# Performance work log

Measured on AMD Instinct MI355X. Metric: run time of the kernel, lower is better.

## Reference

```python
import jax, jax.numpy as jnp
import numpy as np

# Conv config (matches init_kwargs)
STRIDE = (1, 1)
PADDING = ((1, 1), (1, 1))
B, CIN, COUT, H, W = 16, 128, 256, 56, 56
KH, KW = 3, 3


def _conv(x, w):
    # NCHW input, OIHW kernel, zeros padding mode
    return jax.lax.conv_general_dilated(
        x, w, window_strides=STRIDE, padding=PADDING,
        dimension_numbers=("NCHW", "OIHW", "NCHW"))


def setup_inputs() -> dict:
    key = jax.random.key(0)
    ks = jax.random.split(key, 6)
    x = jax.random.normal(ks[0], (B, CIN, H, W), dtype=jnp.float32)
    # quantized weight: integer-valued floats (output of module.Q.quantize)
    weight = jnp.round(jax.random.normal(ks[1], (COUT, CIN, KH, KW), dtype=jnp.float32) * 4.0)
    act_s = jnp.asarray(0.0625, dtype=jnp.float32)   # exp2(log_act_s)
    act_q = jnp.asarray(16.0, dtype=jnp.float32)     # exp2(log_act_q)
    azp = jnp.asarray(-4.0, dtype=jnp.float32)       # rounded act zero point (scaled by guard_a)
    wzp = jnp.round(jax.random.normal(ks[2], (COUT,), dtype=jnp.float32) * 2.0)
    fp_scale = (jax.random.uniform(ks[3], (1, COUT, 1, 1), dtype=jnp.float32) + 0.5) * 1e-3
    # bias_full has spatial extent [1, COUT, H_out, W_out]
    bias = jax.random.normal(ks[4], (1, COUT, H, W), dtype=jnp.float32) * 0.1
    guard_a = jnp.asarray(2.0, dtype=jnp.float32)    # 2**act_guard_bit
    guard_w = jnp.asarray(2.0, dtype=jnp.float32)    # 2**weight_guard_bit
    return {"x": x, "weight": weight, "act_s": act_s, "act_q": act_q,
            "azp": azp, "wzp": wzp, "fp_scale": fp_scale, "bias": bias,
            "guard_a": guard_a, "guard_w": guard_w}


def reference(x, weight, act_s, act_q, azp, wzp, fp_scale, bias, guard_a, guard_w):
    # 1) Activation quantization: clamp to quant range then round to integer grid.
    zp = azp * act_s / guard_a
    xq = jnp.clip(x, zp, zp + act_q - act_s)
    xq = guard_a * jnp.round((xq - zp) / act_s)
    # 2) Main integer conv with quantized weights.
    c1 = _conv(xq, weight)
    # 3) Ones-kernel conv: output is identical across all COUT channels,
    #    so compute once as channel-sum followed by a single-channel box conv.
    s = jnp.sum(xq, axis=1, keepdims=True)  # [B, 1, H, W]
    ones_k = jnp.ones((1, 1) + weight.shape[2:], dtype=x.dtype)
    c2 = _conv(s, ones_k)  # [B, 1, H_out, W_out], broadcasts over channels
    # 4) Affine dequant + spatially-varying bias epilogue.
    out = guard_w * c1 + wzp[None, :, None, None] * c2
    return out * fp_scale + bias
```

## Files before the change

kernel.cpp:

```cpp
#include <hip/hip_runtime.h>

#define B_    16
#define CIN_  128
#define COUT_ 256
#define H_    56
#define W_    56
#define YP    58
#define XP    64

typedef int   i32x4 __attribute__((ext_vector_type(4)));
typedef float f4    __attribute__((ext_vector_type(4)));

#define AS_SZ 8192
#define BH_SZ 24704

__device__ __forceinline__ void gload16(const void* g, void* l) {
    __builtin_amdgcn_global_load_lds(
        (const __attribute__((address_space(1))) unsigned int*)g,
        (__attribute__((address_space(3))) unsigned int*)l,
        16, 0, 0);
}

__global__ __launch_bounds__(256) void k_prep(
    const float* __restrict__ x, const float* __restrict__ w,
    const float* __restrict__ p_act_s, const float* __restrict__ p_act_q,
    const float* __restrict__ p_azp,  const float* __restrict__ p_guard_a,
    signed char* __restrict__ xqU, signed char* __restrict__ wt,
    float* __restrict__ s_pad, float* __restrict__ Wsum)
{
    int t = threadIdx.x;
    int blk = blockIdx.x;

    if (blk < 928) {
        int b = blk / YP, y = blk - b * YP;
        __shared__ signed char shq[W_ * 144];
        signed char* orow = xqU + (size_t)blk * XP * CIN_;

        if (y == 0 || y == YP - 1) {
            i32x4 pv = {(int)0x80808080, (int)0x80808080,
                        (int)0x80808080, (int)0x80808080};
            *(i32x4*)(orow + t * 32)      = pv;
            *(i32x4*)(orow + t * 32 + 16) = pv;
            if (t < XP) s_pad[(size_t)blk * XP + t] = 0.0f;
            return;
        }
        int h = y - 1;
        float act_s = p_act_s[0], act_q = p_act_q[0];
        float azp = p_azp[0], ga = p_guard_a[0];
        float zp = azp * act_s / ga;
        float hi = zp + act_q - act_s;
        float inv_s = 1.0f / act_s;

        for (int i = 0; i < 28; ++i) {
            int e = i * 256 + t;
            int cin = e / 56;
            int ww = e - cin * 56;
            float v = x[(((size_t)b * CIN_ + cin) * H_ + h) * W_ + ww];
            v = fminf(fmaxf(v, zp), hi);
            float r = rintf((v - zp) * inv_s);
            float uq = rintf(ga * r * 0.5f) - 128.0f;
            shq[ww * 144 + cin] = (signed char)(int)uq;
        }
        __syncthreads();
        #pragma unroll
        for (int i = 0; i < 2; ++i) {
            int T = i * 256 + t;
            int xx = T >> 3;
            int c16 = T & 7;
            union { i32x4 v; signed char c[16]; } u;
            if (xx >= 1 && xx <= W_) {
                u.v = *(const i32x4*)(shq + (xx - 1) * 144 + c16 * 16);
            } else {
                u.v = (i32x4){(int)0x80808080, (int)0x80808080,
                              (int)0x80808080, (int)0x80808080};
            }
            *(i32x4*)(orow + (size_t)xx * CIN_ + c16 * 16) = u.v;
            int sum = 0;
            #pragma unroll
            for (int j = 0; j < 16; ++j) sum += (int)u.c[j];
            sum += __shfl_xor(sum, 1);
            sum += __shfl_xor(sum, 2);
            sum += __shfl_xor(sum, 4);
            if (c16 == 0)
                s_pad[(size_t)blk * XP + xx] = (float)(2 * sum + 32768);
        }
        return;
    }

    if (blk < 1216) {
        int o = ((blk - 928) * 256 + t) * 4;
        int tile = o >> 13;
        int m    = (o >> 6) & 127;
        int kk   = o & 63;
        int cb = tile & 1, cc = (tile >> 1) & 1, g = tile >> 2;
        int cout = cb * 128 + m;
        int cin0 = cc * 64 + kk;
        int dy = g / 3, dx = g - dy * 3;
        union { int v; signed char c[4]; } pk;
        #pragma unroll
        for (int j = 0; j < 4; ++j) {
            float v = w[(size_t)cout * 1152 + (cin0 + j) * 9 + dy * 3 + dx];
            pk.c[j] = (signed char)(int)v;
        }
        *(int*)(wt + o) = pk.v;
        return;
    }

    {
        int bw = blk - 1216;
        int cout = bw * 16 + (t >> 4);
        int part = t & 15;
        const float* base = w + (size_t)cout * 1152 + part * 72;
        float s = 0.f;
        for (int j = 0; j < 72; ++j) s += base[j];
        s += __shfl_xor(s, 1);
        s += __shfl_xor(s, 2);
        s += __shfl_xor(s, 4);
        s += __shfl_xor(s, 8);
        if (part == 0) Wsum[cout] = s;
        return;
    }
}

__global__ __launch_bounds__(256, 2) void k_gemm(
    const signed char* __restrict__ xqU,
    const signed char* __restrict__ wt,
    const float* __restrict__ s_pad,
    const float* __restrict__ Wsum,
    const float* __restrict__ wzp,
    const float* __restrict__ fps,
    const float* __restrict__ bias,
    const float* __restrict__ p_gw,
    float* __restrict__ out)
{
    __shared__ __align__(16) signed char As[2][AS_SZ];
    __shared__ __align__(16) signed char Bh[2][BH_SZ];
    __shared__ float c2s[4 * 56];

    int tid = threadIdx.x;
    int wv = tid >> 6, lane = tid & 63;
    int xl = lane & 15, q = lane >> 4;
    int p = blockIdx.x, cb = blockIdx.y;
    int b = p / 14, hp = p - b * 14;
    int h = hp * 4;
    int wm0 = (wv >> 1) * 64, wn0 = (wv & 1) * 128;

    if (tid < 224) {
        int rr = tid / 56, wp = tid - rr * 56;
        const float* sp = s_pad + ((size_t)(b * YP + h + rr)) * XP + wp;
        float a = 0.f;
        #pragma unroll
        for (int dy = 0; dy < 3; ++dy)
            #pragma unroll
            for (int dx = 0; dx < 3; ++dx)
                a += sp[dy * XP + dx];
        c2s[tid] = a;
    }

    i32x4 acc[4][8];
    #pragma unroll
    for (int mi = 0; mi < 4; ++mi)
        #pragma unroll
        for (int ni = 0; ni < 8; ++ni)
            acc[mi][ni] = (i32x4){0, 0, 0, 0};

    const signed char* xb = xqU + (size_t)(b * YP + h) * XP * CIN_;

    int a_base = (wm0 + xl) * 64 + q * 16;
    int bn_base[8];
    #pragma unroll
    for (int ni = 0; ni < 8; ++ni) {
        int n = wn0 + ni * 16 + xl;
        int rn = n >> 6, wp = n & 63;
        bn_base[ni] = (rn * XP + wp) * 64 + q * 16;
    }

    #define STAGE_A(buf_, g_, cc_)                                          \
        {                                                                   \
            const signed char* wsrc = wt + (size_t)((((g_)*2+(cc_))*2)+cb) * 8192; \
            signed char* dstb = As[buf_];                                   \
            _Pragma("unroll")                                               \
            for (int r_ = 0; r_ < 2; ++r_)                                  \
                gload16(wsrc + (r_ * 256 + tid) * 16,                       \
                        dstb + (r_ * 256 + wv * 64) * 16);                  \
        }
    #define STAGE_B(buf_, cc_)                                              \
        {                                                                   \
            signed char* dstb = Bh[buf_];                                   \
            _Pragma("unroll")                                               \
            for (int r_ = 0; r_ < 6; ++r_) {                                \
                int T_ = r_ * 256 + tid;                                    \
                int p_ = T_ & 3;                                            \
                int x_ = (T_ >> 2) & 63;                                    \
                int yy_ = T_ >> 8;                                          \
                gload16(xb + (size_t)(yy_ * XP + x_) * CIN_ + (cc_) * 64 + p_ * 16, \
                        dstb + (r_ * 256 + wv * 64) * 16);                  \
            }                                                               \
        }

    STAGE_A(0, 0, 0)
    STAGE_B(0, 0)
    __syncthreads();

    for (int i = 0; i < 18; ++i) {
        int cc = (i >= 9) ? 1 : 0;
        int g = i - cc * 9;
        if (i < 17) {
            int gn = g + 1, ccn = cc;
            if (gn == 9) { gn = 0; ccn = 1; }
            STAGE_A((i + 1) & 1, gn, ccn)
            if (gn == 0) STAGE_B(1, 1)
        }
        {
            const signed char* Ab = As[i & 1];
            const signed char* Bb = Bh[cc];
            int dy = g / 3, dx = g - dy * 3;
            int boff = dy * (XP * 64) + dx * 64;
            i32x4 af[4], bfr[8];
            #pragma unroll
            for (int mi = 0; mi < 4; ++mi)
                af[mi] = *(const i32x4*)(Ab + a_base + mi * 1024);
            #pragma unroll
            for (int ni = 0; ni < 8; ++ni)
                bfr[ni] = *(const i32x4*)(Bb + bn_base[ni] + boff);
            #pragma unroll
            for (int mi = 0; mi < 4; ++mi)
                #pragma unroll
                for (int ni = 0; ni < 8; ++ni)
                    acc[mi][ni] = __builtin_amdgcn_mfma_i32_16x16x64_i8(
                        af[mi], bfr[ni], acc[mi][ni], 0, 0, 0);
        }
        __syncthreads();
    }

    float gw = p_gw[0];
    #pragma unroll
    for (int mi = 0; mi < 4; ++mi) {
        #pragma unroll
        for (int r = 0; r < 4; ++r) {
            int cout = cb * 128 + wm0 + mi * 16 + q * 4 + r;
            float wz = wzp[cout], fs = fps[cout], ws = Wsum[cout];
            #pragma unroll
            for (int ni = 0; ni < 8; ++ni) {
                int n = wn0 + ni * 16 + xl;
                int wp = n & 63;
                if (wp < W_) {
                    int rn = n >> 6;
                    int hrow = h + rn;
                    float c1 = 2.0f * (float)acc[mi][ni][r] + 256.0f * ws;
                    float v = gw * c1 + wz * c2s[rn * 56 + wp];
                    out[(((size_t)b * COUT_ + cout) * H_ + hrow) * W_ + wp] =
                        v * fs + bias[((size_t)cout * H_ + hrow) * W_ + wp];
                }
            }
        }
    }
}

extern "C" void kernel_launch(void* const* d_in, const int* in_sizes, int n_in,
                              void* d_out, int out_size, void* d_ws, size_t ws_size,
                              hipStream_t stream)
{
    const float* x     = (const float*)d_in[0];
    const float* wht   = (const float*)d_in[1];
    const float* act_s = (const float*)d_in[2];
    const float* act_q = (const float*)d_in[3];
    const float* azp   = (const float*)d_in[4];
    const float* wzp   = (const float*)d_in[5];
    const float* fps   = (const float*)d_in[6];
    const float* bias  = (const float*)d_in[7];
    const float* ga    = (const float*)d_in[8];
    const float* gw    = (const float*)d_in[9];
    float* out = (float*)d_out;

    char* ws = (char*)d_ws;
    signed char* xqU  = (signed char*)(ws);
    signed char* wt   = (signed char*)(ws + 7602176);
    float*       spad = (float*)(ws + 7602176 + 294912);
    float*       Wsum = (float*)(ws + 7602176 + 294912 + 237568);

    k_prep<<<dim3(1232), dim3(256), 0, stream>>>(
        x, wht, act_s, act_q, azp, ga, xqU, wt, spad, Wsum);
    k_gemm<<<dim3(224, 2), dim3(256), 0, stream>>>(
        xqU, wt, spad, Wsum, wzp, fps, bias, gw, out);
}
```

Before: 141.5 us.

## Load weights directly from global in MFMA fragment layout, shrink tile to two rows

After: 150.2 us. +6.2%, slower.

```diff
diff --git a/kernel.cpp b/kernel.cpp
--- a/kernel.cpp
+++ b/kernel.cpp
@@ -10,9 +10,6 @@
 
 typedef int   i32x4 __attribute__((ext_vector_type(4)));
 typedef float f4    __attribute__((ext_vector_type(4)));
-
-#define AS_SZ 8192
-#define BH_SZ 24704
 
 __device__ __forceinline__ void gload16(const void* g, void* l) {
     __builtin_amdgcn_global_load_lds(
@@ -89,19 +86,21 @@
 
     if (blk < 1216) {
         int o = ((blk - 928) * 256 + t) * 4;
-        int tile = o >> 13;
-        int m    = (o >> 6) & 127;
-        int kk   = o & 63;
-        int cb = tile & 1, cc = (tile >> 1) & 1, g = tile >> 2;
-        int cout = cb * 128 + m;
-        int cin0 = cc * 64 + kk;
+        int i_  = o >> 14;
+        int cc  = (i_ >= 9) ? 1 : 0;
+        int g   = i_ - cc * 9;
+        int cbp = (o >> 13) & 1;
+        int mh  = (o >> 12) & 1;
+        int mi  = (o >> 10) & 3;
+        int ln  = (o >> 4) & 63;
+        int cout = cbp * 128 + mh * 64 + mi * 16 + (ln & 15);
+        int cin0 = cc * 64 + (ln >> 4) * 16 + (o & 15);
         int dy = g / 3, dx = g - dy * 3;
+        const float* src = w + (size_t)cout * 1152 + cin0 * 9 + dy * 3 + dx;
         union { int v; signed char c[4]; } pk;
         #pragma unroll
-        for (int j = 0; j < 4; ++j) {
-            float v = w[(size_t)cout * 1152 + (cin0 + j) * 9 + dy * 3 + dx];
-            pk.c[j] = (signed char)(int)v;
-        }
+        for (int j = 0; j < 4; ++j)
+            pk.c[j] = (signed char)(int)src[j * 9];
         *(int*)(wt + o) = pk.v;
         return;
     }
@@ -122,7 +121,7 @@
     }
 }
 
-__global__ __launch_bounds__(256, 2) void k_gemm(
+__global__ __launch_bounds__(256, 3) void k_gemm(
     const signed char* __restrict__ xqU,
     const signed char* __restrict__ wt,
     const float* __restrict__ s_pad,
@@ -133,19 +132,20 @@
     const float* __restrict__ p_gw,
     float* __restrict__ out)
 {
-    __shared__ __align__(16) signed char As[2][AS_SZ];
-    __shared__ __align__(16) signed char Bh[2][BH_SZ];
-    __shared__ float c2s[4 * 56];
+    __shared__ __align__(16) signed char Bh[2 * 16384 + 128];
+    __shared__ float c2s[2 * 56];
 
     int tid = threadIdx.x;
     int wv = tid >> 6, lane = tid & 63;
     int xl = lane & 15, q = lane >> 4;
-    int p = blockIdx.x, cb = blockIdx.y;
-    int b = p / 14, hp = p - b * 14;
-    int h = hp * 4;
-    int wm0 = (wv >> 1) * 64, wn0 = (wv & 1) * 128;
-
-    if (tid < 224) {
+    int p = (blockIdx.x & 7) * 56 + (blockIdx.x >> 3);
+    int cb = blockIdx.y;
+    int b = p / 28, hp = p - b * 28;
+    int h = hp * 2;
+    int mh = wv >> 1;
+    int rn = wv & 1;
+
+    if (tid < 112) {
         int rr = tid / 56, wp = tid - rr * 56;
         const float* sp = s_pad + ((size_t)(b * YP + h + rr)) * XP + wp;
         float a = 0.f;
@@ -157,96 +157,85 @@
         c2s[tid] = a;
     }
 
-    i32x4 acc[4][8];
+    const signed char* xb = xqU + (size_t)(b * YP + h) * XP * CIN_;
+    #pragma unroll
+    for (int cc = 0; cc < 2; ++cc)
+        #pragma unroll
+        for (int r_ = 0; r_ < 4; ++r_) {
+            int T_ = r_ * 256 + tid;
+            int p_ = T_ & 3;
+            int x_ = (T_ >> 2) & 63;
+            int yy_ = T_ >> 8;
+            gload16(xb + (size_t)(yy_ * XP + x_) * CIN_ + cc * 64 + p_ * 16,
+                    Bh + cc * 16384 + (r_ * 256 + wv * 64) * 16);
+        }
+
+    i32x4 acc[4][4];
     #pragma unroll
     for (int mi = 0; mi < 4; ++mi)
         #pragma unroll
-        for (int ni = 0; ni < 8; ++ni)
+        for (int ni = 0; ni < 4; ++ni)
             acc[mi][ni] = (i32x4){0, 0, 0, 0};
 
-    const signed char* xb = xqU + (size_t)(b * YP + h) * XP * CIN_;
-
-    int a_base = (wm0 + xl) * 64 + q * 16;
-    int bn_base[8];
-    #pragma unroll
-    for (int ni = 0; ni < 8; ++ni) {
-        int n = wn0 + ni * 16 + xl;
-        int rn = n >> 6, wp = n & 63;
-        bn_base[ni] = (rn * XP + wp) * 64 + q * 16;
-    }
-
-    #define STAGE_A(buf_, g_, cc_)                                          \
-        {                                                                   \
-            const signed char* wsrc = wt + (size_t)((((g_)*2+(cc_))*2)+cb) * 8192; \
-            signed char* dstb = As[buf_];                                   \
-            _Pragma("unroll")                                               \
-            for (int r_ = 0; r_ < 2; ++r_)                                  \
-                gload16(wsrc + (r_ * 256 + tid) * 16,                       \
-                        dstb + (r_ * 256 + wv * 64) * 16);                  \
-        }
-    #define STAGE_B(buf_, cc_)                                              \
-        {                                                                   \
-            signed char* dstb = Bh[buf_];                                   \
-            _Pragma("unroll")                                               \
-            for (int r_ = 0; r_ < 6; ++r_) {                                \
-                int T_ = r_ * 256 + tid;                                    \
-                int p_ = T_ & 3;                                            \
-                int x_ = (T_ >> 2) & 63;                                    \
-                int yy_ = T_ >> 8;                                          \
-                gload16(xb + (size_t)(yy_ * XP + x_) * CIN_ + (cc_) * 64 + p_ * 16, \
-                        dstb + (r_ * 256 + wv * 64) * 16);                  \
-            }                                                               \
-        }
-
-    STAGE_A(0, 0, 0)
-    STAGE_B(0, 0)
+    const signed char* aptr = wt + (size_t)(cb * 8192 + mh * 4096) + (size_t)lane * 16;
+    int bn2[4];
+    #pragma unroll
+    for (int ni = 0; ni < 4; ++ni)
+        bn2[ni] = rn * 4096 + (ni * 16 + xl) * 64 + q * 16;
+
+    i32x4 af[2][4], bf[2][4];
+
+    #define LDA(bufv, iv)                                                      \
+        {                                                                      \
+            _Pragma("unroll")                                                  \
+            for (int mi_ = 0; mi_ < 4; ++mi_)                                  \
+                af[bufv][mi_] = *(const i32x4*)(aptr + (iv) * 16384 + mi_ * 1024); \
+        }
+    #define LDB(bufv, iv)                                                      \
+        {                                                                      \
+            const int cc_ = ((iv) >= 9) ? 1 : 0;                               \
+            const int g_ = (iv) - cc_ * 9;                                     \
+            const int dy_ = g_ / 3, dx_ = g_ - dy_ * 3;                        \
+            const int off_ = cc_ * 16384 + dy_ * 4096 + dx_ * 64;              \
+            _Pragma("unroll")                                                  \
+            for (int ni_ = 0; ni_ < 4; ++ni_)                                  \
+                bf[bufv][ni_] = *(const i32x4*)(Bh + off_ + bn2[ni_]);         \
+        }
+
+    LDA(0, 0)
     __syncthreads();
-
+    LDB(0, 0)
+
+    #pragma unroll
     for (int i = 0; i < 18; ++i) {
-        int cc = (i >= 9) ? 1 : 0;
-        int g = i - cc * 9;
+        const int cur = i & 1, nxt = cur ^ 1;
         if (i < 17) {
-            int gn = g + 1, ccn = cc;
-            if (gn == 9) { gn = 0; ccn = 1; }
-            STAGE_A((i + 1) & 1, gn, ccn)
-            if (gn == 0) STAGE_B(1, 1)
-        }
-        {
-            const signed char* Ab = As[i & 1];
-            const signed char* Bb = Bh[cc];
-            int dy = g / 3, dx = g - dy * 3;
-            int boff = dy * (XP * 64) + dx * 64;
-            i32x4 af[4], bfr[8];
-            #pragma unroll
-            for (int mi = 0; mi < 4; ++mi)
-                af[mi] = *(const i32x4*)(Ab + a_base + mi * 1024);
-            #pragma unroll
-            for (int ni = 0; ni < 8; ++ni)
-                bfr[ni] = *(const i32x4*)(Bb + bn_base[ni] + boff);
-            #pragma unroll
-            for (int mi = 0; mi < 4; ++mi)
-                #pragma unroll
-                for (int ni = 0; ni < 8; ++ni)
-                    acc[mi][ni] = __builtin_amdgcn_mfma_i32_16x16x64_i8(
-                        af[mi], bfr[ni], acc[mi][ni], 0, 0, 0);
-        }
-        __syncthreads();
-    }
+            LDA(nxt, i + 1)
+            LDB(nxt, i + 1)
+        }
+        #pragma unroll
+        for (int mi = 0; mi < 4; ++mi)
+            #pragma unroll
+            for (int ni = 0; ni < 4; ++ni)
+                acc[mi][ni] = __builtin_amdgcn_mfma_i32_16x16x64_i8(
+                    af[cur][mi], bf[cur][ni], acc[mi][ni], 0, 0, 0);
+    }
+
+    #undef LDA
+    #undef LDB
 
     float gw = p_gw[0];
+    int hrow = h + rn;
     #pragma unroll
     for (int mi = 0; mi < 4; ++mi) {
         #pragma unroll
         for (int r = 0; r < 4; ++r) {
-            int cout = cb * 128 + wm0 + mi * 16 + q * 4 + r;
+            int cout = cb * 128 + mh * 64 + mi * 16 + q * 4 + r;
             float wz = wzp[cout], fs = fps[cout], ws = Wsum[cout];
             #pragma unroll
-            for (int ni = 0; ni < 8; ++ni) {
-                int n = wn0 + ni * 16 + xl;
-                int wp = n & 63;
+            for (int ni = 0; ni < 4; ++ni) {
+                int wp = ni * 16 + xl;
                 if (wp < W_) {
-                    int rn = n >> 6;
-                    int hrow = h + rn;
                     float c1 = 2.0f * (float)acc[mi][ni][r] + 256.0f * ws;
                     float v = gw * c1 + wz * c2s[rn * 56 + wp];
                     out[(((size_t)b * COUT_ + cout) * H_ + hrow) * W_ + wp] =
@@ -281,6 +270,6 @@
 
     k_prep<<<dim3(1232), dim3(256), 0, stream>>>(
         x, wht, act_s, act_q, azp, ga, xqU, wt, spad, Wsum);
-    k_gemm<<<dim3(224, 2), dim3(256), 0, stream>>>(
+    k_gemm<<<dim3(448, 2), dim3(256), 0, stream>>>(
         xqU, wt, spad, Wsum, wzp, fps, bias, gw, out);
 }
```
